# Kernel tuning notes

Hardware: AMD Instinct MI355X
Metric: run time of the kernel (lower is better)

The kernel has to match this reference:

```python
import jax, jax.numpy as jnp
import numpy as np

B, V, D = 4096, 20, 768


def _conv1d_k3(x, w, b):
    # x: [B, V, D]; single-channel conv1d, kernel=3, padding=1 (torch cross-correlation)
    xp = jnp.pad(x, ((0, 0), (0, 0), (1, 1)))
    return w[0] * xp[..., :-2] + w[1] * xp[..., 1:-1] + w[2] * xp[..., 2:] + b[0]


def setup_inputs() -> dict:
    key = jax.random.key(0)
    ks = jax.random.split(key, 10)
    s = 0.02  # small init scale for weights
    return {
        "text_features": jax.random.normal(ks[0], (B, D), jnp.float32),
        "viewport_features": jax.random.normal(ks[1], (B, V, D), jnp.float32),
        "W1": jax.random.normal(ks[2], (D, D), jnp.float32) * s,
        "b1": jax.random.normal(ks[3], (D,), jnp.float32) * s,
        "W2": jax.random.normal(ks[4], (D, D), jnp.float32) * s,
        "b2": jax.random.normal(ks[5], (D,), jnp.float32) * s,
        "cw1": jax.random.normal(ks[6], (3,), jnp.float32) * 0.5,
        "cb1": jax.random.normal(ks[7], (1,), jnp.float32) * 0.1,
        "cw2": jax.random.normal(ks[8], (3,), jnp.float32) * 0.5,
        "cb2": jax.random.normal(ks[9], (1,), jnp.float32) * 0.1,
    }


def reference(text_features, viewport_features, W1, b1, W2, b2, cw1, cb1, cw2, cb2):
    # Batched over all 20 viewports at once (original loops over i).
    fli_norm = jax.nn.softmax(viewport_features, axis=-1)          # [B,V,D]
    # torch Linear: x @ W.T + b
    m1 = jnp.einsum('bvd,ed->bve', fli_norm, W1) + b1              # mlp1(fli_norm)
    m2 = jnp.einsum('bvd,ed->bve', fli_norm, W2) + b2              # mlp2(fli_norm)
    fused = jax.nn.relu(text_features[:, None, :] * m1 + m2)       # [B,V,D]
    fused = _conv1d_k3(fused, cw1, cb1)
    fused = jax.nn.relu(fused)
    fused = _conv1d_k3(fused, cw2, cb2)
    return fused.reshape(B, V * D)                                 # torch.cat along dim=1
```

## Files before the change

### kernel.cpp

```cpp
#include <hip/hip_runtime.h>

typedef unsigned short u16;
typedef unsigned char u8;
typedef __attribute__((ext_vector_type(8))) short short8;
typedef __attribute__((ext_vector_type(4))) float f32x4;

#define Bn 4096
#define Vn 20
#define Dn 768
#define Mn (Bn * Vn)
#define Nn (2 * Dn)

#define BM 256
#define BNt 256
#define NTILES (Nn / BNt)
#define GRID ((Mn / BM) * NTILES)
#define PANEL (256 * Dn)

#define SCL 32.0f
#define ISCL2 (1.0f / 1024.0f)

typedef __attribute__((address_space(1))) void GV;
typedef __attribute__((address_space(3))) void LV;

__device__ __forceinline__ u16 f2bf(float f) {
  union { float f; unsigned u; } v; v.f = f;
  unsigned r = v.u + 0x7FFFu + ((v.u >> 16) & 1u);
  return (u16)(r >> 16);
}
__device__ __forceinline__ float bf2f(u16 x) {
  union { unsigned u; float f; } v; v.u = ((unsigned)x) << 16; return v.f;
}


__global__ __launch_bounds__(512) void softmax_k(const float* __restrict__ vf,
                                                 u8* __restrict__ X8) {
  __shared__ __align__(16) u8 lds[24576];
  const int t = threadIdx.x;
  const int r = t >> 4;
  const int g = t & 15;
  const size_t q = (size_t)blockIdx.x * 32 + r;
  const float* src = vf + q * Dn + g * 4;
  float4 v[12];
  #pragma unroll
  for (int u = 0; u < 12; ++u) v[u] = *(const float4*)(src + u * 64);
  float mx = -1e30f;
  #pragma unroll
  for (int u = 0; u < 12; ++u)
    mx = fmaxf(mx, fmaxf(fmaxf(v[u].x, v[u].y), fmaxf(v[u].z, v[u].w)));
  #pragma unroll
  for (int off = 1; off < 16; off <<= 1) mx = fmaxf(mx, __shfl_xor(mx, off));
  float s = 0.f;
  #pragma unroll
  for (int u = 0; u < 12; ++u) {
    v[u].x = __expf(v[u].x - mx); v[u].y = __expf(v[u].y - mx);
    v[u].z = __expf(v[u].z - mx); v[u].w = __expf(v[u].w - mx);
    s += (v[u].x + v[u].y) + (v[u].z + v[u].w);
  }
  #pragma unroll
  for (int off = 1; off < 16; off <<= 1) s += __shfl_xor(s, off);
  const float inv = SCL / s;
  const int base = ((g >> 1) & 3) * 256 + (r >> 1) * 16 + (r & 1) * 8 + (g & 1) * 4;
  #pragma unroll
  for (int u = 0; u < 12; ++u) {
    unsigned pk = 0;
    pk = __builtin_amdgcn_cvt_pk_fp8_f32(v[u].x * inv, v[u].y * inv, pk, false);
    pk = __builtin_amdgcn_cvt_pk_fp8_f32(v[u].z * inv, v[u].w * inv, pk, true);
    *(unsigned*)(lds + ((g >> 3) + 2 * u) * 1024 + base) = pk;
  }
  __syncthreads();
  u8* dst = X8 + (size_t)(blockIdx.x >> 3) * PANEL + (blockIdx.x & 7) * 256;
  #pragma unroll
  for (int rd = 0; rd < 3; ++rd) {
    const int o = (rd * 512 + t) * 16;
    *(uint4*)(dst + (o >> 10) * 8192 + ((o >> 8) & 3) * 2048 + (o & 255)) =
        *(const uint4*)(lds + o);
  }
}

__global__ __launch_bounds__(256) void build_wt_k(const float* __restrict__ W1,
                                                  const float* __restrict__ W2,
                                                  u8* __restrict__ Wt8) {
  int idx = blockIdx.x * 256 + threadIdx.x;
  if (idx >= Dn * (Dn / 4)) return;
  int j = idx / (Dn / 4), d4 = (idx - j * (Dn / 4)) * 4;
  int b = j >> 5, c = j & 31;
  float4 a = *(const float4*)(W1 + (size_t)j * Dn + d4);
  float4 e = *(const float4*)(W2 + (size_t)j * Dn + d4);
  unsigned p1 = 0, p2 = 0;
  p1 = __builtin_amdgcn_cvt_pk_fp8_f32(a.x * SCL, a.y * SCL, p1, false);
  p1 = __builtin_amdgcn_cvt_pk_fp8_f32(a.z * SCL, a.w * SCL, p1, true);
  p2 = __builtin_amdgcn_cvt_pk_fp8_f32(e.x * SCL, e.y * SCL, p2, false);
  p2 = __builtin_amdgcn_cvt_pk_fp8_f32(e.z * SCL, e.w * SCL, p2, true);
  const int slice = d4 >> 5, plane = (d4 >> 3) & 3, bb = d4 & 7;
  const int j1 = b * 64 + c, j2 = b * 64 + 32 + c;
  const int q1 = j1 & 255, q2 = j2 & 255;
  *(unsigned*)(Wt8 + (size_t)(j1 >> 8) * PANEL + (size_t)slice * 8192
               + plane * 2048 + (q1 >> 1) * 16 + (q1 & 1) * 8 + bb) = p1;
  *(unsigned*)(Wt8 + (size_t)(j2 >> 8) * PANEL + (size_t)slice * 8192
               + plane * 2048 + (q2 >> 1) * 16 + (q2 & 1) * 8 + bb) = p2;
}

__global__ __launch_bounds__(512, 2) void gemm_fuse_k(
    const u8* __restrict__ X8, const u8* __restrict__ Wt8,
    const float* __restrict__ b1, const float* __restrict__ b2,
    const float* __restrict__ text, float* __restrict__ out,
    u16* __restrict__ seam,
    const float* __restrict__ cw1, const float* __restrict__ cb1,
    const float* __restrict__ cw2, const float* __restrict__ cb2) {
  __shared__ __align__(16) u16 smem[65536];
  u8* smem8 = (u8*)smem;

  const int h = blockIdx.x;
  const int lin = (h & 7) * (GRID / 8) + (h >> 3);
  const int by = lin / NTILES, bx = lin - by * NTILES;
  const int brow = by * BM;

  const int t = threadIdx.x, w = t >> 6, l = t & 63;
  const int lo = l & 15, hi = l >> 4;
  const int wrr = w >> 2, wcc = w & 3;

  int offA[8], offB[4];
  #pragma unroll
  for (int m = 0; m < 8; ++m)
    offA[m] = hi * 2048 + (wrr * 64 + m * 8 + (lo >> 1)) * 16 + (lo & 1) * 8;
  #pragma unroll
  for (int n = 0; n < 4; ++n)
    offB[n] = hi * 2048 + (wcc * 32 + n * 8 + (lo >> 1)) * 16 + (lo & 1) * 8;

  const u8* gAp = X8 + (size_t)by * PANEL + t * 16;
  const u8* gBp = Wt8 + (size_t)bx * PANEL + t * 16;

#define STG_A(DST, SL) __builtin_amdgcn_global_load_lds( \
    (GV*)(gAp + (size_t)(SL) * 8192), (LV*)(smem8 + (DST) + w * 1024), 16, 0, 0)
#define STG_B(DST, SL) __builtin_amdgcn_global_load_lds( \
    (GV*)(gBp + (size_t)(SL) * 8192), (LV*)(smem8 + (DST) + w * 1024), 16, 0, 0)

  STG_A(0, 0);              STG_B(16384, 0);
  STG_A(32768, 2);          STG_B(49152, 2);
  STG_A(8192, 1);           STG_B(24576, 1);
  STG_A(40960, 3);          STG_B(57344, 3);
  asm volatile("s_waitcnt vmcnt(6)" ::: "memory");
  __builtin_amdgcn_s_barrier();

  f32x4 acc[8][4] = {};
  long af[8], bb0, bb1;

#define PH(SB, KH, NH, NEWA, STG, VM) do {                                     \
    if (NEWA) { _Pragma("unroll") for (int m = 0; m < 8; ++m)                  \
      af[m] = *(const long*)(smem8 + (SB) + (KH) * 8192 + offA[m]); }          \
    bb0 = *(const long*)(smem8 + (SB) + 16384 + (KH) * 8192 + offB[(NH)*2]);   \
    bb1 = *(const long*)(smem8 + (SB) + 16384 + (KH) * 8192 + offB[(NH)*2+1]); \
    STG;                                                                       \
    __builtin_amdgcn_s_barrier();                                              \
    asm volatile("s_waitcnt lgkmcnt(0)" ::: "memory");                         \
    __builtin_amdgcn_sched_barrier(0);                                         \
    __builtin_amdgcn_s_setprio(1);                                             \
    _Pragma("unroll") for (int m = 0; m < 8; ++m) {                            \
      acc[m][(NH)*2]   = __builtin_amdgcn_mfma_f32_16x16x32_fp8_fp8(af[m], bb0, acc[m][(NH)*2],   0, 0, 0); \
      acc[m][(NH)*2+1] = __builtin_amdgcn_mfma_f32_16x16x32_fp8_fp8(af[m], bb1, acc[m][(NH)*2+1], 0, 0, 0); \
    }                                                                          \
    __builtin_amdgcn_s_setprio(0);                                             \
    VM;                                                                        \
    __builtin_amdgcn_s_barrier();                                              \
  } while (0)

#define VM2 asm volatile("s_waitcnt vmcnt(2)" ::: "memory")
#define VM0 asm volatile("s_waitcnt vmcnt(0)" ::: "memory")

  #pragma unroll
  for (int i = 0; i < 6; ++i) {
    const int sa = 2 * (2 * i + 1);
    const int sb = 2 * (2 * i + 2);
    PH(0, 0, 0, true,  if (i >= 1) STG_A(32768, sa),     ;  );
    PH(0, 0, 1, false, if (i >= 1) STG_B(49152, sa),     VM2);
    PH(0, 1, 0, true,  if (i >= 1) STG_A(40960, sa + 1), ;  );
    PH(0, 1, 1, false, if (i >= 1) STG_B(57344, sa + 1), VM2);
    PH(32768, 0, 0, true,  if (i <= 4) STG_A(0, sb),         ;  );
    PH(32768, 0, 1, false, if (i <= 4) STG_B(16384, sb),     if (i == 5) { VM0; } else { VM2; });
    PH(32768, 1, 0, true,  if (i <= 4) STG_A(8192, sb + 1),  ;  );
    PH(32768, 1, 1, false, if (i <= 4) STG_B(24576, sb + 1), if (i <= 4) { VM2; });
  }
#undef PH
#undef VM2
#undef VM0
#undef STG_A
#undef STG_B

  const float w10 = cw1[0], w11 = cw1[1], w12 = cw1[2], c1b = cb1[0];
  const float w20 = cw2[0], w21 = cw2[1], w22 = cw2[2], c2b = cb2[0];

  u16* fsm = smem;
  u16* tsm = smem + 32768;

  #pragma unroll
  for (int n = 0; n < 2; ++n) {
    const int cl = wcc * 32 + n * 16 + lo;
    const int e  = bx * 128 + cl;
    const float B1 = b1[e], B2 = b2[e];
    #pragma unroll
    for (int m = 0; m < 8; ++m) {
      const int rl = wrr * 128 + m * 16 + hi * 4;
      uint2 pk;
      u16* pku = (u16*)&pk;
      #pragma unroll
      for (int r = 0; r < 4; ++r) {
        const int gr = brow + rl + r;
        const float v1 = acc[m][n][r] * ISCL2 + B1;
        const float v2 = acc[m][n + 2][r] * ISCL2 + B2;
        const float tf = text[(size_t)(gr / Vn) * Dn + e];
        pku[r] = f2bf(fmaxf(tf * v1 + v2, 0.0f));
      }
      *(uint2*)(fsm + cl * 256 + (rl ^ ((cl & 31) << 3))) = pk;
      const int sidx = (cl < 4) ? cl : ((cl >= 124) ? cl - 120 : -1);
      if (sidx >= 0)
        *(uint2*)(seam + ((size_t)(by * 6 + bx) * 8 + sidx) * 256 + rl) = pk;
    }
  }
  __syncthreads();

  const int cl = t & 127, rb = t >> 7;
  const int cL = cl ? cl - 1 : 0, cR = (cl < 127) ? cl + 1 : 127;
  short8 tC[8];
  #pragma unroll
  for (int j = 0; j < 8; ++j) {
    const int R = rb * 64 + j * 8;
    short8 sL = *(const short8*)(fsm + cL * 256 + (R ^ ((cL & 31) << 3)));
    short8 sC = *(const short8*)(fsm + cl * 256 + (R ^ ((cl & 31) << 3)));
    short8 sR = *(const short8*)(fsm + cR * 256 + (R ^ ((cR & 31) << 3)));
    short8 o;
    #pragma unroll
    for (int k = 0; k < 8; ++k) {
      float a = bf2f((u16)sL[k]), b = bf2f((u16)sC[k]), c = bf2f((u16)sR[k]);
      float v = fmaxf(fmaf(w10, a, fmaf(w11, b, fmaf(w12, c, c1b))), 0.0f);
      o[k] = (short)f2bf(v);
    }
    *(short8*)(tsm + cl * 256 + (R ^ ((cl & 31) << 3))) = o;
    tC[j] = o;
  }
  __syncthreads();

  const bool wr_ok = (cl >= 2 && cl <= 125);
  #pragma unroll
  for (int j = 0; j < 8; ++j) {
    const int R = rb * 64 + j * 8;
    short8 tL = *(const short8*)(tsm + cL * 256 + (R ^ ((cL & 31) << 3)));
    short8 tR = *(const short8*)(tsm + cR * 256 + (R ^ ((cR & 31) << 3)));
    #pragma unroll
    for (int k = 0; k < 8; ++k) {
      float v = fmaf(w20, bf2f((u16)tL[k]),
                fmaf(w21, bf2f((u16)tC[j][k]),
                fmaf(w22, bf2f((u16)tR[k]), c2b)));
      if (wr_ok)
        out[(size_t)(brow + R + k) * Dn + bx * 128 + cl] = v;
    }
  }
}

__global__ __launch_bounds__(256) void seam_k(const u16* __restrict__ seam,
                                              float* __restrict__ out,
                                              const float* __restrict__ cw1,
                                              const float* __restrict__ cb1,
                                              const float* __restrict__ cw2,
                                              const float* __restrict__ cb2) {
  const int bid = blockIdx.x;
  const int by = bid / 6, bx = bid - by * 6;
  const int r = threadIdx.x;
  const float w10 = cw1[0], w11 = cw1[1], w12 = cw1[2], c1b = cb1[0];
  const float w20 = cw2[0], w21 = cw2[1], w22 = cw2[2], c2b = cb2[0];
  #define SM(B, I) bf2f(seam[((size_t)(B) * 8 + (I)) * 256 + r])
  float fm2 = 0.f, fm1 = 0.f, fR0 = 0.f, fR1 = 0.f;
  if (bx > 0) { fm2 = SM(bid - 1, 6); fm1 = SM(bid - 1, 7); }
  if (bx < 5) { fR0 = SM(bid + 1, 0); fR1 = SM(bid + 1, 1); }
  const float f0 = SM(bid, 0), f1 = SM(bid, 1), f2 = SM(bid, 2), f3 = SM(bid, 3);
  const float f124 = SM(bid, 4), f125 = SM(bid, 5), f126 = SM(bid, 6), f127 = SM(bid, 7);
  #undef SM
  #define C1(a, b, c) fmaxf(fmaf(w10, (a), fmaf(w11, (b), fmaf(w12, (c), c1b))), 0.0f)
  const float tm1  = (bx > 0) ? C1(fm2, fm1, f0) : 0.0f;
  const float t0   = C1(fm1, f0, f1);
  const float t1   = C1(f0, f1, f2);
  const float t2   = C1(f1, f2, f3);
  const float t125 = C1(f124, f125, f126);
  const float t126 = C1(f125, f126, f127);
  const float t127 = C1(f126, f127, fR0);
  const float t128 = (bx < 5) ? C1(f127, fR0, fR1) : 0.0f;
  #undef C1
  const size_t go = (size_t)(by * 256 + r) * Dn + bx * 128;
  out[go + 0]   = fmaf(w20, tm1,  fmaf(w21, t0,   fmaf(w22, t1,   c2b)));
  out[go + 1]   = fmaf(w20, t0,   fmaf(w21, t1,   fmaf(w22, t2,   c2b)));
  out[go + 126] = fmaf(w20, t125, fmaf(w21, t126, fmaf(w22, t127, c2b)));
  out[go + 127] = fmaf(w20, t126, fmaf(w21, t127, fmaf(w22, t128, c2b)));
}

extern "C" void kernel_launch(void* const* d_in, const int* in_sizes, int n_in,
                              void* d_out, int out_size, void* d_ws, size_t ws_size,
                              hipStream_t stream) {
  const float* text = (const float*)d_in[0];
  const float* vf   = (const float*)d_in[1];
  const float* W1   = (const float*)d_in[2];
  const float* b1   = (const float*)d_in[3];
  const float* W2   = (const float*)d_in[4];
  const float* b2   = (const float*)d_in[5];
  const float* cw1  = (const float*)d_in[6];
  const float* cb1  = (const float*)d_in[7];
  const float* cw2  = (const float*)d_in[8];
  const float* cb2  = (const float*)d_in[9];
  float* out = (float*)d_out;

  u8*  X8   = (u8*)d_ws;
  u8*  Wt8  = X8 + (size_t)Mn * Dn;
  u16* seam = (u16*)(Wt8 + (size_t)Nn * Dn);

  softmax_k<<<Mn / 32, 512, 0, stream>>>(vf, X8);
  build_wt_k<<<(Dn * (Dn / 4) + 255) / 256, 256, 0, stream>>>(W1, W2, Wt8);
  gemm_fuse_k<<<GRID, 512, 0, stream>>>(X8, Wt8, b1, b2, text, out, seam,
                                        cw1, cb1, cw2, cb2);
  seam_k<<<GRID, 256, 0, stream>>>(seam, out, cw1, cb1, cw2, cb2);
}
```

Before: 336.9 us.

## Switch FP8 GEMM to 16-byte LDS fragments with triple-buffered 64-K stages

Changes the packed FP8 layout of activations and weights so each lane reads 16 bytes (two K-steps) per LDS load instead of 8 bytes. The main loop becomes 12 iterations over 64-wide K tiles, rotating through three LDS buffers with loads issued two tiles ahead. Each iteration runs two MFMA phases, one per pair of N columns. The aim is fewer LDS read instructions and fewer barriers per unit of MFMA work, plus deeper prefetch. The cost is changed bank-conflict behaviour and more live registers for fragments.

```diff
diff --git a/kernel.cpp b/kernel.cpp
--- a/kernel.cpp
+++ b/kernel.cpp
@@ -4,6 +4,7 @@
 typedef unsigned char u8;
 typedef __attribute__((ext_vector_type(8))) short short8;
 typedef __attribute__((ext_vector_type(4))) float f32x4;
+typedef __attribute__((ext_vector_type(2))) long long2v;
 
 #define Bn 4096
 #define Vn 20
@@ -60,20 +61,21 @@
   #pragma unroll
   for (int off = 1; off < 16; off <<= 1) s += __shfl_xor(s, off);
   const float inv = SCL / s;
-  const int base = ((g >> 1) & 3) * 256 + (r >> 1) * 16 + (r & 1) * 8 + (g & 1) * 4;
+  const int base = ((g >> 1) & 3) * 512 + r * 16 + (g >> 3) * 8 + (g & 1) * 4;
   #pragma unroll
   for (int u = 0; u < 12; ++u) {
     unsigned pk = 0;
     pk = __builtin_amdgcn_cvt_pk_fp8_f32(v[u].x * inv, v[u].y * inv, pk, false);
     pk = __builtin_amdgcn_cvt_pk_fp8_f32(v[u].z * inv, v[u].w * inv, pk, true);
-    *(unsigned*)(lds + ((g >> 3) + 2 * u) * 1024 + base) = pk;
+    *(unsigned*)(lds + u * 2048 + base) = pk;
   }
   __syncthreads();
-  u8* dst = X8 + (size_t)(blockIdx.x >> 3) * PANEL + (blockIdx.x & 7) * 256;
+  u8* dst = X8 + (size_t)(blockIdx.x >> 3) * PANEL + (blockIdx.x & 7) * 512;
   #pragma unroll
   for (int rd = 0; rd < 3; ++rd) {
     const int o = (rd * 512 + t) * 16;
-    *(uint4*)(dst + (o >> 10) * 8192 + ((o >> 8) & 3) * 2048 + (o & 255)) =
+    const int chunk = o >> 9;
+    *(uint4*)(dst + (chunk >> 2) * 16384 + (chunk & 3) * 4096 + (o & 511)) =
         *(const uint4*)(lds + o);
   }
 }
@@ -92,13 +94,11 @@
   p1 = __builtin_amdgcn_cvt_pk_fp8_f32(a.z * SCL, a.w * SCL, p1, true);
   p2 = __builtin_amdgcn_cvt_pk_fp8_f32(e.x * SCL, e.y * SCL, p2, false);
   p2 = __builtin_amdgcn_cvt_pk_fp8_f32(e.z * SCL, e.w * SCL, p2, true);
-  const int slice = d4 >> 5, plane = (d4 >> 3) & 3, bb = d4 & 7;
+  const size_t off = (size_t)(d4 >> 6) * 16384 + ((d4 >> 3) & 3) * 4096
+                   + ((d4 >> 5) & 1) * 8 + (d4 & 7);
   const int j1 = b * 64 + c, j2 = b * 64 + 32 + c;
-  const int q1 = j1 & 255, q2 = j2 & 255;
-  *(unsigned*)(Wt8 + (size_t)(j1 >> 8) * PANEL + (size_t)slice * 8192
-               + plane * 2048 + (q1 >> 1) * 16 + (q1 & 1) * 8 + bb) = p1;
-  *(unsigned*)(Wt8 + (size_t)(j2 >> 8) * PANEL + (size_t)slice * 8192
-               + plane * 2048 + (q2 >> 1) * 16 + (q2 & 1) * 8 + bb) = p2;
+  *(unsigned*)(Wt8 + (size_t)(j1 >> 8) * PANEL + off + (j1 & 255) * 16) = p1;
+  *(unsigned*)(Wt8 + (size_t)(j2 >> 8) * PANEL + off + (j2 & 255) * 16) = p2;
 }
 
 __global__ __launch_bounds__(512, 2) void gemm_fuse_k(
@@ -123,67 +123,78 @@
   int offA[8], offB[4];
   #pragma unroll
   for (int m = 0; m < 8; ++m)
-    offA[m] = hi * 2048 + (wrr * 64 + m * 8 + (lo >> 1)) * 16 + (lo & 1) * 8;
+    offA[m] = hi * 4096 + (wrr * 128 + m * 16 + lo) * 16;
   #pragma unroll
   for (int n = 0; n < 4; ++n)
-    offB[n] = hi * 2048 + (wcc * 32 + n * 8 + (lo >> 1)) * 16 + (lo & 1) * 8;
+    offB[n] = 16384 + hi * 4096 + (wcc * 64 + n * 16 + lo) * 16;
 
   const u8* gAp = X8 + (size_t)by * PANEL + t * 16;
   const u8* gBp = Wt8 + (size_t)bx * PANEL + t * 16;
 
-#define STG_A(DST, SL) __builtin_amdgcn_global_load_lds( \
-    (GV*)(gAp + (size_t)(SL) * 8192), (LV*)(smem8 + (DST) + w * 1024), 16, 0, 0)
-#define STG_B(DST, SL) __builtin_amdgcn_global_load_lds( \
-    (GV*)(gBp + (size_t)(SL) * 8192), (LV*)(smem8 + (DST) + w * 1024), 16, 0, 0)
-
-  STG_A(0, 0);              STG_B(16384, 0);
-  STG_A(32768, 2);          STG_B(49152, 2);
-  STG_A(8192, 1);           STG_B(24576, 1);
-  STG_A(40960, 3);          STG_B(57344, 3);
-  asm volatile("s_waitcnt vmcnt(6)" ::: "memory");
+#define STG_A(SB, T) do {                                                      \
+    __builtin_amdgcn_global_load_lds((GV*)(gAp + (size_t)(T) * 16384),         \
+        (LV*)(smem8 + (SB) + w * 1024), 16, 0, 0);                             \
+    __builtin_amdgcn_global_load_lds((GV*)(gAp + (size_t)(T) * 16384 + 8192),  \
+        (LV*)(smem8 + (SB) + 8192 + w * 1024), 16, 0, 0); } while (0)
+#define STG_B(SB, T) do {                                                      \
+    __builtin_amdgcn_global_load_lds((GV*)(gBp + (size_t)(T) * 16384),         \
+        (LV*)(smem8 + (SB) + 16384 + w * 1024), 16, 0, 0);                     \
+    __builtin_amdgcn_global_load_lds((GV*)(gBp + (size_t)(T) * 16384 + 8192),  \
+        (LV*)(smem8 + (SB) + 24576 + w * 1024), 16, 0, 0); } while (0)
+
+  STG_A(0, 0);     STG_B(0, 0);
+  STG_A(32768, 1); STG_B(32768, 1);
+  asm volatile("s_waitcnt vmcnt(4)" ::: "memory");
   __builtin_amdgcn_s_barrier();
 
   f32x4 acc[8][4] = {};
-  long af[8], bb0, bb1;
-
-#define PH(SB, KH, NH, NEWA, STG, VM) do {                                     \
-    if (NEWA) { _Pragma("unroll") for (int m = 0; m < 8; ++m)                  \
-      af[m] = *(const long*)(smem8 + (SB) + (KH) * 8192 + offA[m]); }          \
-    bb0 = *(const long*)(smem8 + (SB) + 16384 + (KH) * 8192 + offB[(NH)*2]);   \
-    bb1 = *(const long*)(smem8 + (SB) + 16384 + (KH) * 8192 + offB[(NH)*2+1]); \
-    STG;                                                                       \
-    __builtin_amdgcn_s_barrier();                                              \
-    asm volatile("s_waitcnt lgkmcnt(0)" ::: "memory");                         \
-    __builtin_amdgcn_sched_barrier(0);                                         \
-    __builtin_amdgcn_s_setprio(1);                                             \
-    _Pragma("unroll") for (int m = 0; m < 8; ++m) {                            \
-      acc[m][(NH)*2]   = __builtin_amdgcn_mfma_f32_16x16x32_fp8_fp8(af[m], bb0, acc[m][(NH)*2],   0, 0, 0); \
-      acc[m][(NH)*2+1] = __builtin_amdgcn_mfma_f32_16x16x32_fp8_fp8(af[m], bb1, acc[m][(NH)*2+1], 0, 0, 0); \
-    }                                                                          \
-    __builtin_amdgcn_s_setprio(0);                                             \
-    VM;                                                                        \
-    __builtin_amdgcn_s_barrier();                                              \
-  } while (0)
-
-#define VM2 asm volatile("s_waitcnt vmcnt(2)" ::: "memory")
-#define VM0 asm volatile("s_waitcnt vmcnt(0)" ::: "memory")
-
-  #pragma unroll
-  for (int i = 0; i < 6; ++i) {
-    const int sa = 2 * (2 * i + 1);
-    const int sb = 2 * (2 * i + 2);
-    PH(0, 0, 0, true,  if (i >= 1) STG_A(32768, sa),     ;  );
-    PH(0, 0, 1, false, if (i >= 1) STG_B(49152, sa),     VM2);
-    PH(0, 1, 0, true,  if (i >= 1) STG_A(40960, sa + 1), ;  );
-    PH(0, 1, 1, false, if (i >= 1) STG_B(57344, sa + 1), VM2);
-    PH(32768, 0, 0, true,  if (i <= 4) STG_A(0, sb),         ;  );
-    PH(32768, 0, 1, false, if (i <= 4) STG_B(16384, sb),     if (i == 5) { VM0; } else { VM2; });
-    PH(32768, 1, 0, true,  if (i <= 4) STG_A(8192, sb + 1),  ;  );
-    PH(32768, 1, 1, false, if (i <= 4) STG_B(24576, sb + 1), if (i <= 4) { VM2; });
-  }
-#undef PH
-#undef VM2
-#undef VM0
+  long2v af[8], bb0, bb1;
+
+  #pragma unroll
+  for (int T = 0; T < 12; ++T) {
+    const int cs = (T % 3) * 32768;
+    const int ss = ((T + 2) % 3) * 32768;
+    const bool st = (T <= 9);
+
+    #pragma unroll
+    for (int m = 0; m < 8; ++m)
+      af[m] = *(const long2v*)(smem8 + cs + offA[m]);
+    bb0 = *(const long2v*)(smem8 + cs + offB[0]);
+    bb1 = *(const long2v*)(smem8 + cs + offB[1]);
+    if (st) STG_A(ss, T + 2);
+    __builtin_amdgcn_s_barrier();
+    asm volatile("s_waitcnt lgkmcnt(0)" ::: "memory");
+    __builtin_amdgcn_sched_barrier(0);
+    __builtin_amdgcn_s_setprio(1);
+    #pragma unroll
+    for (int m = 0; m < 8; ++m) {
+      acc[m][0] = __builtin_amdgcn_mfma_f32_16x16x32_fp8_fp8(af[m][0], bb0[0], acc[m][0], 0, 0, 0);
+      acc[m][0] = __builtin_amdgcn_mfma_f32_16x16x32_fp8_fp8(af[m][1], bb0[1], acc[m][0], 0, 0, 0);
+      acc[m][1] = __builtin_amdgcn_mfma_f32_16x16x32_fp8_fp8(af[m][0], bb1[0], acc[m][1], 0, 0, 0);
+      acc[m][1] = __builtin_amdgcn_mfma_f32_16x16x32_fp8_fp8(af[m][1], bb1[1], acc[m][1], 0, 0, 0);
+    }
+    __builtin_amdgcn_s_setprio(0);
+    __builtin_amdgcn_s_barrier();
+
+    bb0 = *(const long2v*)(smem8 + cs + offB[2]);
+    bb1 = *(const long2v*)(smem8 + cs + offB[3]);
+    if (st) STG_B(ss, T + 2);
+    __builtin_amdgcn_s_barrier();
+    asm volatile("s_waitcnt lgkmcnt(0)" ::: "memory");
+    __builtin_amdgcn_sched_barrier(0);
+    __builtin_amdgcn_s_setprio(1);
+    #pragma unroll
+    for (int m = 0; m < 8; ++m) {
+      acc[m][2] = __builtin_amdgcn_mfma_f32_16x16x32_fp8_fp8(af[m][0], bb0[0], acc[m][2], 0, 0, 0);
+      acc[m][2] = __builtin_amdgcn_mfma_f32_16x16x32_fp8_fp8(af[m][1], bb0[1], acc[m][2], 0, 0, 0);
+      acc[m][3] = __builtin_amdgcn_mfma_f32_16x16x32_fp8_fp8(af[m][0], bb1[0], acc[m][3], 0, 0, 0);
+      acc[m][3] = __builtin_amdgcn_mfma_f32_16x16x32_fp8_fp8(af[m][1], bb1[1], acc[m][3], 0, 0, 0);
+    }
+    __builtin_amdgcn_s_setprio(0);
+    if (T <= 9)       asm volatile("s_waitcnt vmcnt(4)" ::: "memory");
+    else if (T == 10) asm volatile("s_waitcnt vmcnt(0)" ::: "memory");
+    __builtin_amdgcn_s_barrier();
+  }
 #undef STG_A
 #undef STG_B
 
```

New measurement: 326.1 us. 3.2% less time.
